# Optimization experiments

Measured on AMD Instinct MI355X. Metric: run time of the kernel, lower is better.

The kernel has to match this reference:

```python
import jax, jax.numpy as jnp
import numpy as np

NODE_DIM, EDGE_DIM, HIDDEN, OUT_DIM, HEADS = 128, 64, 128, 64, 4
N_NODES, N_EDGES = 4096, 16384
EPS = 1e-8


def setup_inputs() -> dict:
    key = jax.random.key(0)
    ks = jax.random.split(key, 10)
    s = lambda *shape: 1.0 / np.sqrt(shape[-2] if len(shape) > 1 else shape[-1])
    return {
        "node_features": jax.random.normal(ks[0], (N_NODES, NODE_DIM), jnp.float32),
        "incidence_matrix": jax.random.uniform(ks[1], (N_NODES, N_EDGES), jnp.float32),
        # per-head node_transform: [H, node_dim, hidden]
        "W1": jax.random.normal(ks[2], (HEADS, NODE_DIM, HIDDEN), jnp.float32) * (1.0 / np.sqrt(NODE_DIM)),
        "b1": jnp.zeros((HEADS, HIDDEN), jnp.float32),
        # per-head attention_weight: Linear(hidden, 1) -> vector [H, hidden]
        "Wa": jax.random.normal(ks[3], (HEADS, HIDDEN), jnp.float32) * (1.0 / np.sqrt(HIDDEN)),
        "ba": jnp.zeros((HEADS,), jnp.float32),
        # per-head expand_output: [H, hidden, edge_dim]
        "W2": jax.random.normal(ks[4], (HEADS, HIDDEN, EDGE_DIM), jnp.float32) * (1.0 / np.sqrt(HIDDEN)),
        "b2": jnp.zeros((HEADS, EDGE_DIM), jnp.float32),
        # output_transform: [H*edge_dim, output_dim]
        "Wout": jax.random.normal(ks[5], (HEADS * EDGE_DIM, OUT_DIM), jnp.float32) * (1.0 / np.sqrt(HEADS * EDGE_DIM)),
        "bout": jnp.zeros((OUT_DIM,), jnp.float32),
    }


def _min_max_normalize(x):
    # per-column min-max over the edge axis (axis=-2)
    mn = jnp.min(x, axis=-2, keepdims=True)
    mx = jnp.max(x, axis=-2, keepdims=True)
    return (x - mn) / (mx - mn + EPS)


def reference(node_features, incidence_matrix, W1, b1, Wa, ba, W2, b2, Wout, bout):
    # transformed node features per head: [H, N, hidden]
    t = jnp.einsum("nd,hdk->hnk", node_features, W1) + b1[:, None, :]
    # incidence^T @ t -> masked edge features: [H, E, hidden]
    m = jnp.einsum("ne,hnk->hek", incidence_matrix, t)
    # attention scores: [H, E]
    scores = jnp.einsum("hek,hk->he", m, Wa) + ba[:, None]
    scores = jax.nn.leaky_relu(scores, negative_slope=0.2)
    # softmax over edges (dim=0 of [E,1] per head)
    coeffs = jax.nn.softmax(scores, axis=-1)  # [H, E]
    w = coeffs[:, :, None] * m  # [H, E, hidden]
    u = jnp.einsum("hek,hko->heo", w, W2) + b2[:, None, :]  # [H, E, edge_dim]
    u = _min_max_normalize(u)
    # concat heads -> [E, H*edge_dim]
    cat = jnp.transpose(u, (1, 0, 2)).reshape(N_EDGES, HEADS * EDGE_DIM)
    cat = jax.nn.relu(cat)  # dropout is identity in eval mode
    return cat @ Wout + bout  # [E, output_dim]
```

## Files before the change

### kernel.cpp

```cpp
#include <hip/hip_runtime.h>
#include <stdint.h>

#define NODES 4096
#define EDGES 16384
#define CSTR  288

typedef __attribute__((ext_vector_type(4))) float    f32x4;
typedef __attribute__((ext_vector_type(8))) short    short8;
typedef __attribute__((ext_vector_type(4))) uint32_t u32x4;
typedef __attribute__((ext_vector_type(4))) unsigned short u16x4;

__device__ __forceinline__ unsigned short f2bf(float f) {
  union { float f; uint32_t u; } v; v.f = f;
  uint32_t u = v.u;
  return (unsigned short)((u + 0x7fffu + ((u >> 16) & 1u)) >> 16);
}
__device__ __forceinline__ float bf2f(unsigned short s) {
  union { uint32_t u; float f; } v; v.u = ((uint32_t)s) << 16;
  return v.f;
}

__global__ __launch_bounds__(256) void k1_prep(
    const float* __restrict__ nf, const float* __restrict__ W1,
    const float* __restrict__ b1, const float* __restrict__ Wa,
    const float* __restrict__ W2, unsigned short* __restrict__ PqT)
{
  __shared__ float nf_s[8][128];
  __shared__ float t_s[8][132];
  __shared__ float p_s[65][8];
  const int n0 = blockIdx.x * 8;
  const int t = threadIdx.x;
  for (int i = 0; i < 4; i++) {
    int idx = t + 256 * i;
    nf_s[idx >> 7][idx & 127] = nf[(size_t)(n0 + (idx >> 7)) * 128 + (idx & 127)];
  }
  for (int h = 0; h < 4; h++) {
    __syncthreads();
    {
      const int k = t & 127, ng = t >> 7;
      float a0 = b1[h * 128 + k], a1 = a0, a2 = a0, a3 = a0;
      const float* w1p = W1 + (size_t)h * 128 * 128 + k;
      for (int d = 0; d < 128; d++) {
        float wv = w1p[(size_t)d * 128];
        a0 += nf_s[ng * 4 + 0][d] * wv;
        a1 += nf_s[ng * 4 + 1][d] * wv;
        a2 += nf_s[ng * 4 + 2][d] * wv;
        a3 += nf_s[ng * 4 + 3][d] * wv;
      }
      t_s[ng * 4 + 0][k] = a0; t_s[ng * 4 + 1][k] = a1;
      t_s[ng * 4 + 2][k] = a2; t_s[ng * 4 + 3][k] = a3;
    }
    __syncthreads();
    {
      const int o = t & 63, ng = t >> 6;
      float a0 = 0.f, a1 = 0.f;
      const float* w2p = W2 + (size_t)h * 128 * 64 + o;
      for (int k = 0; k < 128; k++) {
        float wv = w2p[(size_t)k * 64];
        a0 += t_s[ng * 2 + 0][k] * wv;
        a1 += t_s[ng * 2 + 1][k] * wv;
      }
      p_s[o][ng * 2 + 0] = a0; p_s[o][ng * 2 + 1] = a1;
    }
    if (t < 8) {
      float a = 0.f;
      for (int k = 0; k < 128; k++) a += t_s[t][k] * Wa[h * 128 + k];
      p_s[64][t] = a;
    }
    __syncthreads();
    if (t < 72) {
      unsigned short tmp[8];
      if (t < 64) {
        for (int j = 0; j < 8; j++) tmp[j] = f2bf(p_s[t][j]);
      } else if (t == 64) {
        for (int j = 0; j < 8; j++) tmp[j] = f2bf(p_s[64][j]);
      } else if (t == 65) {
        for (int j = 0; j < 8; j++) {
          unsigned short hi = f2bf(p_s[64][j]);
          tmp[j] = f2bf(p_s[64][j] - bf2f(hi));
        }
      } else {
        for (int j = 0; j < 8; j++) tmp[j] = 0;
      }
      u32x4 pk;
      pk[0] = (uint32_t)tmp[0] | ((uint32_t)tmp[1] << 16);
      pk[1] = (uint32_t)tmp[2] | ((uint32_t)tmp[3] << 16);
      pk[2] = (uint32_t)tmp[4] | ((uint32_t)tmp[5] << 16);
      pk[3] = (uint32_t)tmp[6] | ((uint32_t)tmp[7] << 16);
      *(u32x4*)(&PqT[(size_t)(h * 72 + t) * 4096 + n0]) = pk;
    }
  }
}

__global__ __launch_bounds__(256) void k2_gemm(
    const float* __restrict__ inc, const unsigned short* __restrict__ PqT,
    float* __restrict__ C)
{
  __shared__ unsigned short As[64 * 64];
  __shared__ unsigned short AsLo[64 * 64];
  __shared__ unsigned short Bs[288 * 72];
  const int t = threadIdx.x;
  const int lane = t & 63, w = t >> 6;
  const int wr = w & 1, wc = w >> 1;
  const int e0 = blockIdx.x * 64;
  const int eq = t & 15, kq = t >> 4;

  f32x4 acc[2][9];
  for (int mi = 0; mi < 2; mi++)
    for (int ni = 0; ni < 9; ni++)
      acc[mi][ni] = (f32x4){0.f, 0.f, 0.f, 0.f};

  f32x4 av[4];
  u32x4 bv[9];

  auto load_tiles = [&](int ks) {
    const float* ap = inc + (size_t)(ks * 64 + kq * 4) * 16384 + e0 + eq * 4;
#pragma unroll
    for (int r = 0; r < 4; r++)
      av[r] = *(const f32x4*)(ap + (size_t)r * 16384);
#pragma unroll
    for (int j = 0; j < 9; j++) {
      int f = t + 256 * j; int c = f >> 3, q8 = f & 7;
      bv[j] = *(const u32x4*)(PqT + (size_t)c * 4096 + ks * 64 + q8 * 8);
    }
  };
  auto store_tiles = [&]() {
#pragma unroll
    for (int i = 0; i < 4; i++) {
      int e = 4 * eq + i;
      int p = ((kq >> 1) + eq + 4 * i) & 7;
      u16x4 wv, wl;
      wv[0] = f2bf(av[0][i]); wv[1] = f2bf(av[1][i]);
      wv[2] = f2bf(av[2][i]); wv[3] = f2bf(av[3][i]);
      wl[0] = f2bf(av[0][i] - bf2f(wv[0]));
      wl[1] = f2bf(av[1][i] - bf2f(wv[1]));
      wl[2] = f2bf(av[2][i] - bf2f(wv[2]));
      wl[3] = f2bf(av[3][i] - bf2f(wv[3]));
      *(u16x4*)(&As[e * 64 + p * 8 + (kq & 1) * 4]) = wv;
      *(u16x4*)(&AsLo[e * 64 + p * 8 + (kq & 1) * 4]) = wl;
    }
#pragma unroll
    for (int j = 0; j < 9; j++) {
      int f = t + 256 * j; int c = f >> 3, q8 = f & 7;
      *(u32x4*)(&Bs[c * 72 + q8 * 8]) = bv[j];
    }
  };
  auto compute = [&]() {
#pragma unroll
    for (int ksub = 0; ksub < 2; ksub++) {
      short8 afr[2], aflo[2];
      const int q = lane >> 4;
#pragma unroll
      for (int mi = 0; mi < 2; mi++) {
        int e = wr * 32 + mi * 16 + (lane & 15);
        int p = ((4 * ksub + q) + (e >> 2) + 4 * (e & 3)) & 7;
        afr[mi]  = *(const short8*)(&As[e * 64 + p * 8]);
        aflo[mi] = *(const short8*)(&AsLo[e * 64 + p * 8]);
      }
#pragma unroll
      for (int ni = 0; ni < 9; ni++) {
        int c = wc * 144 + ni * 16 + (lane & 15);
        const short8 bfr = *(const short8*)(&Bs[c * 72 + 32 * ksub + 8 * q]);
        acc[0][ni] = __builtin_amdgcn_mfma_f32_16x16x32_bf16(afr[0], bfr, acc[0][ni], 0, 0, 0);
        acc[1][ni] = __builtin_amdgcn_mfma_f32_16x16x32_bf16(afr[1], bfr, acc[1][ni], 0, 0, 0);
        if (ni == 4 || ni == 8) {
          acc[0][ni] = __builtin_amdgcn_mfma_f32_16x16x32_bf16(aflo[0], bfr, acc[0][ni], 0, 0, 0);
          acc[1][ni] = __builtin_amdgcn_mfma_f32_16x16x32_bf16(aflo[1], bfr, acc[1][ni], 0, 0, 0);
        }
      }
    }
  };

  load_tiles(0);
  for (int ks = 0; ks < 64; ks++) {
    __syncthreads();
    store_tiles();
    __syncthreads();
    if (ks < 63) load_tiles(ks + 1);
    compute();
  }

#pragma unroll
  for (int mi = 0; mi < 2; mi++)
#pragma unroll
    for (int ni = 0; ni < 9; ni++)
#pragma unroll
      for (int r = 0; r < 4; r++) {
        int e = e0 + wr * 32 + mi * 16 + (lane >> 4) * 4 + r;
        int c = wc * 144 + ni * 16 + (lane & 15);
        C[(size_t)e * CSTR + c] = acc[mi][ni][r];
      }
}

__global__ __launch_bounds__(1024) void k3_softmax(
    const float* __restrict__ C, const float* __restrict__ ba,
    float* __restrict__ coeff)
{
  const int h = blockIdx.x, t = threadIdx.x;
  __shared__ float red[16];
  float vals[16];
  float mx = -1e30f;
  const int cb = h * 72 + 64;
#pragma unroll
  for (int i = 0; i < 16; i++) {
    int e = t + 1024 * i;
    float s = C[(size_t)e * CSTR + cb] + C[(size_t)e * CSTR + cb + 1] + ba[h];
    s = (s > 0.f) ? s : 0.2f * s;
    vals[i] = s;
    mx = fmaxf(mx, s);
  }
  for (int off = 32; off > 0; off >>= 1) mx = fmaxf(mx, __shfl_xor(mx, off, 64));
  if ((t & 63) == 0) red[t >> 6] = mx;
  __syncthreads();
  float gmx = red[0];
  for (int i = 1; i < 16; i++) gmx = fmaxf(gmx, red[i]);
  float total = 0.f;
#pragma unroll
  for (int i = 0; i < 16; i++) { vals[i] = expf(vals[i] - gmx); total += vals[i]; }
  __syncthreads();
  for (int off = 32; off > 0; off >>= 1) total += __shfl_xor(total, off, 64);
  if ((t & 63) == 0) red[t >> 6] = total;
  __syncthreads();
  float gs = 0.f;
  for (int i = 0; i < 16; i++) gs += red[i];
  float inv = 1.f / gs;
#pragma unroll
  for (int i = 0; i < 16; i++) coeff[h * 16384 + t + 1024 * i] = vals[i] * inv;
}

__global__ __launch_bounds__(256) void k4_minmax(
    const float* __restrict__ C, const float* __restrict__ coeff,
    float* __restrict__ pmn, float* __restrict__ pmx)
{
  const int t = threadIdx.x, blk = blockIdx.x;
  const int h = t >> 6, o = t & 63, c = h * 72 + o;
  const int e0 = blk * 64;
  float mn = 1e30f, mx = -1e30f;
  for (int e = 0; e < 64; e++) {
    float u = coeff[h * 16384 + e0 + e] * C[(size_t)(e0 + e) * CSTR + c];
    mn = fminf(mn, u); mx = fmaxf(mx, u);
  }
  pmn[blk * 256 + t] = mn; pmx[blk * 256 + t] = mx;
}

__global__ __launch_bounds__(256) void k4_reduce(
    const float* __restrict__ pmn, const float* __restrict__ pmx,
    float* __restrict__ mnv, float* __restrict__ invv)
{
  const int t = threadIdx.x;
  float mn = 1e30f, mx = -1e30f;
  for (int b = 0; b < 256; b++) {
    mn = fminf(mn, pmn[b * 256 + t]);
    mx = fmaxf(mx, pmx[b * 256 + t]);
  }
  mnv[t] = mn;
  invv[t] = 1.f / (mx - mn + 1e-8f);
}

__global__ __launch_bounds__(256) void k5_out(
    const float* __restrict__ C, const float* __restrict__ coeff,
    const float* __restrict__ mnv, const float* __restrict__ invv,
    const float* __restrict__ Wout, const float* __restrict__ bout,
    float* __restrict__ out)
{
  __shared__ float cat[16][256];
  const int t = threadIdx.x;
  const int e0 = blockIdx.x * 16;
  {
    const int h = t >> 6, o = t & 63, c = h * 72 + o;
    const float mn = mnv[t], inv = invv[t];
#pragma unroll
    for (int el = 0; el < 16; el++) {
      float u = coeff[h * 16384 + e0 + el] * C[(size_t)(e0 + el) * CSTR + c];
      float vn = (u - mn) * inv;
      cat[el][t] = vn > 0.f ? vn : 0.f;
    }
  }
  __syncthreads();
  {
    const int od = t & 63, eg = t >> 6;
    float b = bout[od];
    float a0 = b, a1 = b, a2 = b, a3 = b;
    for (int hc = 0; hc < 256; hc++) {
      float wv = Wout[(size_t)hc * 64 + od];
      a0 += cat[eg * 4 + 0][hc] * wv;
      a1 += cat[eg * 4 + 1][hc] * wv;
      a2 += cat[eg * 4 + 2][hc] * wv;
      a3 += cat[eg * 4 + 3][hc] * wv;
    }
    out[(size_t)(e0 + eg * 4 + 0) * 64 + od] = a0;
    out[(size_t)(e0 + eg * 4 + 1) * 64 + od] = a1;
    out[(size_t)(e0 + eg * 4 + 2) * 64 + od] = a2;
    out[(size_t)(e0 + eg * 4 + 3) * 64 + od] = a3;
  }
}

extern "C" void kernel_launch(void* const* d_in, const int* in_sizes, int n_in,
                              void* d_out, int out_size, void* d_ws, size_t ws_size,
                              hipStream_t stream) {
  const float* nf   = (const float*)d_in[0];
  const float* inc  = (const float*)d_in[1];
  const float* W1   = (const float*)d_in[2];
  const float* b1   = (const float*)d_in[3];
  const float* Wa   = (const float*)d_in[4];
  const float* ba   = (const float*)d_in[5];
  const float* W2   = (const float*)d_in[6];
  const float* Wout = (const float*)d_in[8];
  const float* bout = (const float*)d_in[9];
  float* out = (float*)d_out;

  char* ws = (char*)d_ws;
  unsigned short* PqT = (unsigned short*)(ws);
  float* C     = (float*)(ws + 2359296);
  float* coeff = (float*)(ws + 21233664);
  float* pmn   = (float*)(ws + 21495808);
  float* pmx   = (float*)(ws + 21757952);
  float* mnv   = (float*)(ws + 22020096);
  float* invv  = (float*)(ws + 22021120);

  k1_prep<<<512, 256, 0, stream>>>(nf, W1, b1, Wa, W2, PqT);
  k2_gemm<<<256, 256, 0, stream>>>(inc, PqT, C);
  k3_softmax<<<4, 1024, 0, stream>>>(C, ba, coeff);
  k4_minmax<<<256, 256, 0, stream>>>(C, coeff, pmn, pmx);
  k4_reduce<<<1, 256, 0, stream>>>(pmn, pmx, mnv, invv);
  k5_out<<<1024, 256, 0, stream>>>(C, coeff, mnv, invv, Wout, bout, out);
}
```

Before: 554.3 us.

## Fold W1 into W2/Wa weights, write scores compactly, use atomic min-max

Adds a small kernel that precomposes W1 with W2 and Wa (and folds b1 into an effective bias), so the per-node prep becomes a single 128-wide matvec instead of two chained ones. The GEMM epilogue additionally writes the summed hi/lo score columns into a compact per-head buffer, so softmax reads contiguous data instead of strided C columns. The separate min/max reduce kernel is replaced by order-preserving integer atomics, initialized in the softmax kernel, removing one launch. Folding changes rounding order slightly, and the atomics add contention on 256 addresses.

```diff
diff --git a/kernel.cpp b/kernel.cpp
--- a/kernel.cpp
+++ b/kernel.cpp
@@ -19,82 +19,113 @@
   union { uint32_t u; float f; } v; v.u = ((uint32_t)s) << 16;
   return v.f;
 }
+__device__ __forceinline__ uint32_t fenc(float f) {
+  uint32_t u = __float_as_uint(f);
+  return (u >> 31) ? ~u : (u | 0x80000000u);
+}
+__device__ __forceinline__ float fdec(uint32_t k) {
+  return (k & 0x80000000u) ? __uint_as_float(k ^ 0x80000000u) : __uint_as_float(~k);
+}
+
+__global__ __launch_bounds__(128) void k0_fold(
+    const float* __restrict__ W1, const float* __restrict__ W2,
+    const float* __restrict__ Wa, const float* __restrict__ b1,
+    float* __restrict__ WeT, float* __restrict__ beff)
+{
+  const int h = blockIdx.x / 65, oi = blockIdx.x % 65;
+  const int d = threadIdx.x;
+  const float* W1r = W1 + (size_t)h * 16384 + (size_t)d * 128;
+  float acc = 0.f, p;
+  if (oi < 64) {
+    const float* w2c = W2 + (size_t)h * 8192 + oi;
+#pragma unroll 8
+    for (int kc = 0; kc < 32; kc++) {
+      f32x4 wv = *(const f32x4*)(W1r + kc * 4);
+      acc += wv[0] * w2c[(size_t)(kc * 4 + 0) * 64];
+      acc += wv[1] * w2c[(size_t)(kc * 4 + 1) * 64];
+      acc += wv[2] * w2c[(size_t)(kc * 4 + 2) * 64];
+      acc += wv[3] * w2c[(size_t)(kc * 4 + 3) * 64];
+    }
+    p = b1[h * 128 + d] * w2c[(size_t)d * 64];
+  } else {
+    const float* wac = Wa + h * 128;
+#pragma unroll 8
+    for (int kc = 0; kc < 32; kc++) {
+      f32x4 wv = *(const f32x4*)(W1r + kc * 4);
+      f32x4 av = *(const f32x4*)(wac + kc * 4);
+      acc += wv[0] * av[0] + wv[1] * av[1] + wv[2] * av[2] + wv[3] * av[3];
+    }
+    p = b1[h * 128 + d] * wac[d];
+  }
+  WeT[(size_t)h * 9216 + (size_t)d * 72 + oi] = acc;
+  for (int off = 32; off > 0; off >>= 1) p += __shfl_down(p, off, 64);
+  __shared__ float r2s[2];
+  if ((d & 63) == 0) r2s[d >> 6] = p;
+  __syncthreads();
+  if (d == 0) beff[h * 72 + oi] = r2s[0] + r2s[1];
+}
 
 __global__ __launch_bounds__(256) void k1_prep(
-    const float* __restrict__ nf, const float* __restrict__ W1,
-    const float* __restrict__ b1, const float* __restrict__ Wa,
-    const float* __restrict__ W2, unsigned short* __restrict__ PqT)
-{
-  __shared__ float nf_s[8][128];
-  __shared__ float t_s[8][132];
-  __shared__ float p_s[65][8];
+    const float* __restrict__ nf, const float* __restrict__ WeT,
+    const float* __restrict__ beff, unsigned short* __restrict__ PqT)
+{
+  __shared__ float nf_s[8][132];
   const int n0 = blockIdx.x * 8;
   const int t = threadIdx.x;
-  for (int i = 0; i < 4; i++) {
-    int idx = t + 256 * i;
-    nf_s[idx >> 7][idx & 127] = nf[(size_t)(n0 + (idx >> 7)) * 128 + (idx & 127)];
-  }
-  for (int h = 0; h < 4; h++) {
-    __syncthreads();
-    {
-      const int k = t & 127, ng = t >> 7;
-      float a0 = b1[h * 128 + k], a1 = a0, a2 = a0, a3 = a0;
-      const float* w1p = W1 + (size_t)h * 128 * 128 + k;
-      for (int d = 0; d < 128; d++) {
-        float wv = w1p[(size_t)d * 128];
-        a0 += nf_s[ng * 4 + 0][d] * wv;
-        a1 += nf_s[ng * 4 + 1][d] * wv;
-        a2 += nf_s[ng * 4 + 2][d] * wv;
-        a3 += nf_s[ng * 4 + 3][d] * wv;
-      }
-      t_s[ng * 4 + 0][k] = a0; t_s[ng * 4 + 1][k] = a1;
-      t_s[ng * 4 + 2][k] = a2; t_s[ng * 4 + 3][k] = a3;
-    }
-    __syncthreads();
-    {
-      const int o = t & 63, ng = t >> 6;
-      float a0 = 0.f, a1 = 0.f;
-      const float* w2p = W2 + (size_t)h * 128 * 64 + o;
-      for (int k = 0; k < 128; k++) {
-        float wv = w2p[(size_t)k * 64];
-        a0 += t_s[ng * 2 + 0][k] * wv;
-        a1 += t_s[ng * 2 + 1][k] * wv;
-      }
-      p_s[o][ng * 2 + 0] = a0; p_s[o][ng * 2 + 1] = a1;
-    }
-    if (t < 8) {
-      float a = 0.f;
-      for (int k = 0; k < 128; k++) a += t_s[t][k] * Wa[h * 128 + k];
-      p_s[64][t] = a;
-    }
-    __syncthreads();
-    if (t < 72) {
-      unsigned short tmp[8];
-      if (t < 64) {
-        for (int j = 0; j < 8; j++) tmp[j] = f2bf(p_s[t][j]);
-      } else if (t == 64) {
-        for (int j = 0; j < 8; j++) tmp[j] = f2bf(p_s[64][j]);
-      } else if (t == 65) {
-        for (int j = 0; j < 8; j++) {
-          unsigned short hi = f2bf(p_s[64][j]);
-          tmp[j] = f2bf(p_s[64][j] - bf2f(hi));
-        }
-      } else {
-        for (int j = 0; j < 8; j++) tmp[j] = 0;
-      }
-      u32x4 pk;
-      pk[0] = (uint32_t)tmp[0] | ((uint32_t)tmp[1] << 16);
-      pk[1] = (uint32_t)tmp[2] | ((uint32_t)tmp[3] << 16);
-      pk[2] = (uint32_t)tmp[4] | ((uint32_t)tmp[5] << 16);
-      pk[3] = (uint32_t)tmp[6] | ((uint32_t)tmp[7] << 16);
-      *(u32x4*)(&PqT[(size_t)(h * 72 + t) * 4096 + n0]) = pk;
-    }
+  {
+    int row = t >> 5, col = (t * 4) & 127;
+    *(f32x4*)&nf_s[row][col] = *(const f32x4*)(nf + (size_t)(n0 + row) * 128 + col);
+  }
+  __syncthreads();
+  const int h = t >> 6, o = t & 63;
+  const float* wp = WeT + (size_t)h * 9216 + o;
+  float acc[8];
+  {
+    float b = beff[h * 72 + o];
+#pragma unroll
+    for (int n = 0; n < 8; n++) acc[n] = b;
+  }
+  for (int dc = 0; dc < 32; dc++) {
+    f32x4 nv[8];
+#pragma unroll
+    for (int n = 0; n < 8; n++) nv[n] = *(const f32x4*)&nf_s[n][dc * 4];
+#pragma unroll
+    for (int i = 0; i < 4; i++) {
+      float wv = wp[(size_t)(dc * 4 + i) * 72];
+#pragma unroll
+      for (int n = 0; n < 8; n++) acc[n] += nv[n][i] * wv;
+    }
+  }
+  {
+    unsigned short b[8];
+#pragma unroll
+    for (int n = 0; n < 8; n++) b[n] = f2bf(acc[n]);
+    u32x4 pk;
+    pk[0] = (uint32_t)b[0] | ((uint32_t)b[1] << 16);
+    pk[1] = (uint32_t)b[2] | ((uint32_t)b[3] << 16);
+    pk[2] = (uint32_t)b[4] | ((uint32_t)b[5] << 16);
+    pk[3] = (uint32_t)b[6] | ((uint32_t)b[7] << 16);
+    *(u32x4*)(&PqT[(size_t)(h * 72 + o) * 4096 + n0]) = pk;
+  }
+  if (t < 32) {
+    const int qh = t >> 3, qn = t & 7;
+    const float* wq = WeT + (size_t)qh * 9216 + 64;
+    float a = beff[qh * 72 + 64];
+    for (int d = 0; d < 128; d++) a += nf_s[qn][d] * wq[(size_t)d * 72];
+    unsigned short hi = f2bf(a);
+    unsigned short lo = f2bf(a - bf2f(hi));
+    PqT[(size_t)(qh * 72 + 64) * 4096 + n0 + qn] = hi;
+    PqT[(size_t)(qh * 72 + 65) * 4096 + n0 + qn] = lo;
+  }
+  if (t < 96) {
+    const int ph = t / 24, pr = (t / 4) % 6, pn = (t & 3) * 2;
+    *(uint32_t*)&PqT[(size_t)(ph * 72 + 66 + pr) * 4096 + n0 + pn] = 0u;
   }
 }
 
 __global__ __launch_bounds__(256) void k2_gemm(
     const float* __restrict__ inc, const unsigned short* __restrict__ PqT,
-    float* __restrict__ C)
+    float* __restrict__ C, float* __restrict__ sbuf)
 {
   __shared__ unsigned short As[64 * 64];
   __shared__ unsigned short AsLo[64 * 64];
@@ -190,21 +221,38 @@
         int c = wc * 144 + ni * 16 + (lane & 15);
         C[(size_t)e * CSTR + c] = acc[mi][ni][r];
       }
+
+  const int l15 = lane & 15;
+#pragma unroll
+  for (int mi = 0; mi < 2; mi++)
+#pragma unroll
+    for (int r = 0; r < 4; r++) {
+      int e = e0 + wr * 32 + mi * 16 + (lane >> 4) * 4 + r;
+      {
+        float v = acc[mi][4][r]; float vp = __shfl_xor(v, 1);
+        if (l15 == 0) sbuf[(wc * 2 + 0) * 16384 + e] = v + vp;
+      }
+      {
+        float v = acc[mi][8][r]; float vp = __shfl_xor(v, 1);
+        if (l15 == 8) sbuf[(wc * 2 + 1) * 16384 + e] = v + vp;
+      }
+    }
 }
 
 __global__ __launch_bounds__(1024) void k3_softmax(
-    const float* __restrict__ C, const float* __restrict__ ba,
-    float* __restrict__ coeff)
+    const float* __restrict__ sbuf, const float* __restrict__ ba,
+    float* __restrict__ coeff, uint32_t* __restrict__ pmn_a,
+    uint32_t* __restrict__ pmx_a)
 {
   const int h = blockIdx.x, t = threadIdx.x;
+  if (t < 64) { pmn_a[h * 64 + t] = 0xFFFFFFFFu; pmx_a[h * 64 + t] = 0u; }
   __shared__ float red[16];
   float vals[16];
   float mx = -1e30f;
-  const int cb = h * 72 + 64;
+  const float bav = ba[h];
 #pragma unroll
   for (int i = 0; i < 16; i++) {
-    int e = t + 1024 * i;
-    float s = C[(size_t)e * CSTR + cb] + C[(size_t)e * CSTR + cb + 1] + ba[h];
+    float s = sbuf[h * 16384 + t + 1024 * i] + bav;
     s = (s > 0.f) ? s : 0.2f * s;
     vals[i] = s;
     mx = fmaxf(mx, s);
@@ -230,7 +278,7 @@
 
 __global__ __launch_bounds__(256) void k4_minmax(
     const float* __restrict__ C, const float* __restrict__ coeff,
-    float* __restrict__ pmn, float* __restrict__ pmx)
+    uint32_t* __restrict__ pmn_a, uint32_t* __restrict__ pmx_a)
 {
   const int t = threadIdx.x, blk = blockIdx.x;
   const int h = t >> 6, o = t & 63, c = h * 72 + o;
@@ -240,26 +288,13 @@
     float u = coeff[h * 16384 + e0 + e] * C[(size_t)(e0 + e) * CSTR + c];
     mn = fminf(mn, u); mx = fmaxf(mx, u);
   }
-  pmn[blk * 256 + t] = mn; pmx[blk * 256 + t] = mx;
-}
-
-__global__ __launch_bounds__(256) void k4_reduce(
-    const float* __restrict__ pmn, const float* __restrict__ pmx,
-    float* __restrict__ mnv, float* __restrict__ invv)
-{
-  const int t = threadIdx.x;
-  float mn = 1e30f, mx = -1e30f;
-  for (int b = 0; b < 256; b++) {
-    mn = fminf(mn, pmn[b * 256 + t]);
-    mx = fmaxf(mx, pmx[b * 256 + t]);
-  }
-  mnv[t] = mn;
-  invv[t] = 1.f / (mx - mn + 1e-8f);
+  atomicMin(&pmn_a[t], fenc(mn));
+  atomicMax(&pmx_a[t], fenc(mx));
 }
 
 __global__ __launch_bounds__(256) void k5_out(
     const float* __restrict__ C, const float* __restrict__ coeff,
-    const float* __restrict__ mnv, const float* __restrict__ invv,
+    const uint32_t* __restrict__ pmn_a, const uint32_t* __restrict__ pmx_a,
     const float* __restrict__ Wout, const float* __restrict__ bout,
     float* __restrict__ out)
 {
@@ -268,7 +303,8 @@
   const int e0 = blockIdx.x * 16;
   {
     const int h = t >> 6, o = t & 63, c = h * 72 + o;
-    const float mn = mnv[t], inv = invv[t];
+    const float mn = fdec(pmn_a[t]);
+    const float inv = 1.f / (fdec(pmx_a[t]) - mn + 1e-8f);
 #pragma unroll
     for (int el = 0; el < 16; el++) {
       float u = coeff[h * 16384 + e0 + el] * C[(size_t)(e0 + el) * CSTR + c];
@@ -311,17 +347,18 @@
 
   char* ws = (char*)d_ws;
   unsigned short* PqT = (unsigned short*)(ws);
-  float* C     = (float*)(ws + 2359296);
-  float* coeff = (float*)(ws + 21233664);
-  float* pmn   = (float*)(ws + 21495808);
-  float* pmx   = (float*)(ws + 21757952);
-  float* mnv   = (float*)(ws + 22020096);
-  float* invv  = (float*)(ws + 22021120);
-
-  k1_prep<<<512, 256, 0, stream>>>(nf, W1, b1, Wa, W2, PqT);
-  k2_gemm<<<256, 256, 0, stream>>>(inc, PqT, C);
-  k3_softmax<<<4, 1024, 0, stream>>>(C, ba, coeff);
-  k4_minmax<<<256, 256, 0, stream>>>(C, coeff, pmn, pmx);
-  k4_reduce<<<1, 256, 0, stream>>>(pmn, pmx, mnv, invv);
-  k5_out<<<1024, 256, 0, stream>>>(C, coeff, mnv, invv, Wout, bout, out);
-}
+  float* C      = (float*)(ws + 2359296);
+  float* coeff  = (float*)(ws + 21233664);
+  float* sbuf   = (float*)(ws + 21495808);
+  float* WeT    = (float*)(ws + 21757952);
+  float* beff   = (float*)(ws + 21905408);
+  uint32_t* pmn_a = (uint32_t*)(ws + 21909504);
+  uint32_t* pmx_a = (uint32_t*)(ws + 21910528);
+
+  k0_fold<<<260, 128, 0, stream>>>(W1, W2, Wa, b1, WeT, beff);
+  k1_prep<<<512, 256, 0, stream>>>(nf, WeT, beff, PqT);
+  k2_gemm<<<256, 256, 0, stream>>>(inc, PqT, C, sbuf);
+  k3_softmax<<<4, 1024, 0, stream>>>(sbuf, ba, coeff, pmn_a, pmx_a);
+  k4_minmax<<<256, 256, 0, stream>>>(C, coeff, pmn_a, pmx_a);
+  k5_out<<<1024, 256, 0, stream>>>(C, coeff, pmn_a, pmx_a, Wout, bout, out);
+}
```

Measured after the change: 464.4 us. 16.2% less time.
